# Kernel optimization log

Hardware: AMD Instinct MI355X
Metric: run time of the kernel (lower is better)

Reference implementation:

```python
import jax, jax.numpy as jnp
import numpy as np

NEG = -9e15
SLOPE = 0.1  # LeakyReLU negative_slope in the torch module

B, N, NFEAT = 4, 2048, 256
NHID, NHEADS, NOUT = 64, 8, 128


def setup_inputs() -> dict:
    key = jax.random.key(0)
    ks = jax.random.split(key, 8)
    x = jax.random.normal(ks[0], (B, N, NFEAT), dtype=jnp.float32)
    adj = jax.random.randint(ks[1], (B, N, N), 0, 2, dtype=jnp.int32)
    s = 0.1
    Wh = jax.random.normal(ks[2], (NHEADS, NFEAT, NHID), dtype=jnp.float32) * s
    ah = jax.random.normal(ks[3], (NHEADS, 2 * NHID), dtype=jnp.float32) * s
    bh = jax.random.normal(ks[4], (NHEADS, NHID), dtype=jnp.float32) * s
    Wo = jax.random.normal(ks[5], (NHID * NHEADS, NOUT), dtype=jnp.float32) * s
    ao = jax.random.normal(ks[6], (2 * NOUT,), dtype=jnp.float32) * s
    bo = jax.random.normal(ks[7], (NOUT,), dtype=jnp.float32) * s
    return {"x": x, "adj": adj, "Wh": Wh, "ah": ah, "bh": bh,
            "Wo": Wo, "ao": ao, "bo": bo}


def _leaky(v):
    return jnp.where(v >= 0, v, SLOPE * v)


def _gat_layer(x, adj, W, a, b):
    # x: [B,N,Fin], W: [Fin,F], a: [2F], b: [F]
    h = jnp.einsum('bnf,fo->bno', x, W)          # [B,N,F]
    F = W.shape[1]
    a1, a2 = a[:F], a[F:]
    s1 = h @ a1                                   # [B,N] (query / row term)
    s2 = h @ a2                                   # [B,N] (key / col term)
    e = _leaky(s1[:, :, None] + s2[:, None, :])   # [B,N,N], avoids a_input blowup
    e = jnp.where(adj > 0, e, NEG)
    att = jax.nn.softmax(e, axis=2)               # [B,N,N]
    h_prime = jnp.einsum('bnm,bmf->bnf', att, h) + b
    return jax.nn.elu(h_prime)


def reference(x, adj, Wh, ah, bh, Wo, ao, bo):
    # per-head layers, vmapped over the head axis of the stacked params
    heads = jax.vmap(lambda W, a, b: _gat_layer(x, adj, W, a, b))(Wh, ah, bh)
    # [H,B,N,F] -> concat heads along feature dim: [B,N,H*F]
    hcat = jnp.transpose(heads, (1, 2, 0, 3)).reshape(x.shape[0], x.shape[1], -1)
    out = _gat_layer(hcat, adj, Wo, ao, bo)
    return jax.nn.relu(out)
```

## Files before the change

### kernel.cpp

```cpp
#include <hip/hip_runtime.h>

constexpr int B_ = 4;
constexpr int N_ = 2048;
constexpr int NFEAT_ = 256;
constexpr int NHEADS_ = 8;
constexpr float SLOPE_ = 0.1f;
constexpr float L2E = 1.4426950408889634f;

typedef __attribute__((ext_vector_type(8))) __fp16 f16x8;
typedef __attribute__((ext_vector_type(4))) __fp16 f16x4;
typedef __attribute__((ext_vector_type(2))) __fp16 f16x2;
typedef __attribute__((ext_vector_type(4))) float f32x4;

__device__ __forceinline__ f16x8 pack8(const float* v) {
  union { f16x2 h2[4]; f16x8 h8; } u;
  u.h2[0] = __builtin_amdgcn_cvt_pkrtz(v[0], v[1]);
  u.h2[1] = __builtin_amdgcn_cvt_pkrtz(v[2], v[3]);
  u.h2[2] = __builtin_amdgcn_cvt_pkrtz(v[4], v[5]);
  u.h2[3] = __builtin_amdgcn_cvt_pkrtz(v[6], v[7]);
  return u.h8;
}
__device__ __forceinline__ f16x4 pack4(float a, float b, float c, float d) {
  union { f16x2 h2[2]; f16x4 h4; } u;
  u.h2[0] = __builtin_amdgcn_cvt_pkrtz(a, b);
  u.h2[1] = __builtin_amdgcn_cvt_pkrtz(c, d);
  return u.h4;
}

__global__ __launch_bounds__(256) void k_prep(
    const int* __restrict__ adj, unsigned short* __restrict__ mask2,
    const float* __restrict__ Wh, __fp16* __restrict__ WhB,
    const float* __restrict__ Wo, __fp16* __restrict__ WoB)
{
  const int bid = blockIdx.x;
  const int l = threadIdx.x & 63;
  if (bid < 4096) {
    const size_t gw = ((size_t)bid * 256 + threadIdx.x) >> 6;
    const int jt = (int)(gw & 31);
    const int ig16 = (int)((gw >> 5) & 127);
    const int b = (int)(gw >> 12);
    const int q = l >> 4, c15 = l & 15;
    const int* base = adj + ((size_t)b * N_ + ig16 * 16) * N_ + jt * 64 + l;
    unsigned int msk = 0;
    #pragma unroll
    for (int r = 0; r < 16; ++r) {
      int a = base[(size_t)r * N_];
      unsigned long long bal = __ballot(a > 0);
      unsigned int v = (unsigned int)((bal >> (q * 8)) & 0xffull)
                     | ((unsigned int)((bal >> (q * 8 + 32)) & 0xffull) << 8);
      if (r == c15) msk = v;
    }
    mask2[gw * 64 + l] = (unsigned short)msk;
  } else if (bid < 4160) {
    int s = (int)(((bid - 4096) * 256 + threadIdx.x) >> 6);
    int h = s >> 5, ks = (s >> 2) & 7, ft = s & 3;
    const float* src = Wh + ((size_t)h * 256 + ks * 32 + (l >> 4) * 8) * 64 + ft * 16 + (l & 15);
    float v[8];
    #pragma unroll
    for (int j = 0; j < 8; ++j) v[j] = src[(size_t)j * 64];
    *(f16x8*)(WhB + (size_t)s * 512 + l * 8) = pack8(v);
  } else {
    int s = (int)(((bid - 4160) * 256 + threadIdx.x) >> 6);
    int ks = s >> 3, ft = s & 7;
    const float* src = Wo + ((size_t)ks * 32 + (l >> 4) * 8) * 128 + ft * 16 + (l & 15);
    float v[8];
    #pragma unroll
    for (int j = 0; j < 8; ++j) v[j] = src[(size_t)j * 128];
    *(f16x8*)(WoB + (size_t)s * 512 + l * 8) = pack8(v);
  }
}

__global__ __launch_bounds__(256, 4) void k_gemm1(
    const float* __restrict__ x, const __fp16* __restrict__ WhB,
    const float* __restrict__ ah,
    __fp16* __restrict__ hB1, float* __restrict__ s1h, float* __restrict__ s2h)
{
  constexpr int XP = 264;
  __shared__ __fp16 xs[16 * XP];
  __shared__ __fp16 hT[512 * 16];

  const int t = threadIdx.x;
  const int bid = blockIdx.x;
  const int b = bid >> 7;
  const int n0 = (bid & 127) * 16;

  {
    int r = t >> 4, k0 = (t & 15) * 16;
    const float* src = x + ((size_t)(b * N_) + n0 + r) * NFEAT_ + k0;
    float v0[8], v1[8];
    *(float4*)&v0[0] = *(const float4*)(src);
    *(float4*)&v0[4] = *(const float4*)(src + 4);
    *(float4*)&v1[0] = *(const float4*)(src + 8);
    *(float4*)&v1[4] = *(const float4*)(src + 12);
    *(f16x8*)&xs[r * XP + k0] = pack8(v0);
    *(f16x8*)&xs[r * XP + k0 + 8] = pack8(v1);
  }
  __syncthreads();

  const int w = t >> 6, l = t & 63;
  const int quad = l >> 4, c15 = l & 15;

  f32x4 acc[8];
  #pragma unroll
  for (int i = 0; i < 8; ++i) acc[i] = (f32x4){0.f, 0.f, 0.f, 0.f};

  for (int ks = 0; ks < 8; ++ks) {
    f16x8 af = *(const f16x8*)&xs[c15 * XP + ks * 32 + quad * 8];
    #pragma unroll
    for (int tt = 0; tt < 8; ++tt) {
      int hl = tt >> 2, ft = tt & 3;
      f16x8 bf = *(const f16x8*)(WhB +
          ((((size_t)(2 * w + hl) * 8 + ks) * 4 + ft) * 512) + l * 8);
      acc[tt] = __builtin_amdgcn_mfma_f32_16x16x32_f16(af, bf, acc[tt], 0, 0, 0);
    }
  }

  #pragma unroll
  for (int hl = 0; hl < 2; ++hl) {
    int head = 2 * w + hl;
    float a1v[4], a2v[4];
    #pragma unroll
    for (int ft = 0; ft < 4; ++ft) {
      a1v[ft] = ah[head * 128 + ft * 16 + c15] * L2E;
      a2v[ft] = ah[head * 128 + 64 + ft * 16 + c15] * L2E;
    }
    #pragma unroll
    for (int r = 0; r < 4; ++r) {
      float v1 = 0.f, v2 = 0.f;
      #pragma unroll
      for (int ft = 0; ft < 4; ++ft) {
        v1 = fmaf(acc[hl * 4 + ft][r], a1v[ft], v1);
        v2 = fmaf(acc[hl * 4 + ft][r], a2v[ft], v2);
      }
      #pragma unroll
      for (int off = 1; off < 16; off <<= 1) {
        v1 += __shfl_xor(v1, off, 64);
        v2 += __shfl_xor(v2, off, 64);
      }
      if (c15 == 0) {
        s1h[(size_t)(b * NHEADS_ + head) * N_ + n0 + quad * 4 + r] = v1;
        s2h[(size_t)(b * NHEADS_ + head) * N_ + n0 + quad * 4 + r] = v2;
      }
    }
  }

  #pragma unroll
  for (int tt = 0; tt < 8; ++tt) {
    int f = (2 * w + (tt >> 2)) * 64 + (tt & 3) * 16 + c15;
    *(f16x4*)&hT[f * 16 + quad * 4] =
        pack4(acc[tt][0], acc[tt][1], acc[tt][2], acc[tt][3]);
  }
  __syncthreads();

  const int base_oct = (n0 >> 3) & 3;
  #pragma unroll
  for (int q = 0; q < 4; ++q) {
    int s = t + q * 256;
    int c15v = s & 15, oct = (s >> 4) & 1, ft = (s >> 5) & 3, head = s >> 7;
    f16x8 v = *(const f16x8*)&hT[(head * 64 + ft * 16 + c15v) * 16 + oct * 8];
    int lane0 = (base_oct + oct) * 16 + c15v;
    *(f16x8*)(hB1 +
        ((((size_t)(b * NHEADS_ + head) * 64 + (n0 >> 5)) * 4 + ft) * 512) + lane0 * 8) = v;
  }
}

__global__ __launch_bounds__(256, 4) void k_gemm2(
    const __fp16* __restrict__ g1, const __fp16* __restrict__ WoB,
    const float* __restrict__ ao,
    __fp16* __restrict__ hB2, float* __restrict__ s1o, float* __restrict__ s2o)
{
  constexpr int GP = 520;
  __shared__ __fp16 gs[16 * GP];
  __shared__ __fp16 hT[128 * 16];
  __shared__ float sd1[4][16], sd2[4][16];

  const int t = threadIdx.x;
  const int bid = blockIdx.x;
  const int b = bid >> 7;
  const int n0 = (bid & 127) * 16;

  {
    int r = t >> 4, k0 = (t & 15) * 32;
    const __fp16* src = g1 + ((size_t)(b * N_) + n0 + r) * 512 + k0;
    #pragma unroll
    for (int i = 0; i < 4; ++i)
      *(f16x8*)&gs[r * GP + k0 + i * 8] = *(const f16x8*)(src + i * 8);
  }
  __syncthreads();

  const int w = t >> 6, l = t & 63;
  const int quad = l >> 4, c15 = l & 15;

  f32x4 acc[2];
  acc[0] = (f32x4){0.f, 0.f, 0.f, 0.f};
  acc[1] = (f32x4){0.f, 0.f, 0.f, 0.f};

  for (int ks = 0; ks < 16; ++ks) {
    f16x8 af = *(const f16x8*)&gs[c15 * GP + ks * 32 + quad * 8];
    #pragma unroll
    for (int tt = 0; tt < 2; ++tt) {
      int ft = 2 * w + tt;
      f16x8 bf = *(const f16x8*)(WoB + (((size_t)ks * 8 + ft) * 512) + l * 8);
      acc[tt] = __builtin_amdgcn_mfma_f32_16x16x32_f16(af, bf, acc[tt], 0, 0, 0);
    }
  }

  {
    float a1v[2], a2v[2];
    #pragma unroll
    for (int tt = 0; tt < 2; ++tt) {
      int f = (2 * w + tt) * 16 + c15;
      a1v[tt] = ao[f] * L2E;
      a2v[tt] = ao[128 + f] * L2E;
    }
    #pragma unroll
    for (int r = 0; r < 4; ++r) {
      float v1 = acc[0][r] * a1v[0] + acc[1][r] * a1v[1];
      float v2 = acc[0][r] * a2v[0] + acc[1][r] * a2v[1];
      #pragma unroll
      for (int off = 1; off < 16; off <<= 1) {
        v1 += __shfl_xor(v1, off, 64);
        v2 += __shfl_xor(v2, off, 64);
      }
      if (c15 == 0) { sd1[w][quad * 4 + r] = v1; sd2[w][quad * 4 + r] = v2; }
    }
  }

  #pragma unroll
  for (int tt = 0; tt < 2; ++tt) {
    int f = (2 * w + tt) * 16 + c15;
    *(f16x4*)&hT[f * 16 + quad * 4] =
        pack4(acc[tt][0], acc[tt][1], acc[tt][2], acc[tt][3]);
  }
  __syncthreads();

  if (t < 16)
    s1o[(size_t)b * N_ + n0 + t] = sd1[0][t] + sd1[1][t] + sd1[2][t] + sd1[3][t];
  else if (t < 32) {
    int rr = t - 16;
    s2o[(size_t)b * N_ + n0 + rr] = sd2[0][rr] + sd2[1][rr] + sd2[2][rr] + sd2[3][rr];
  }

  {
    int c15v = t & 15, oct = (t >> 4) & 1, ft = t >> 5;
    f16x8 v = *(const f16x8*)&hT[(ft * 16 + c15v) * 16 + oct * 8];
    int base_oct = (n0 >> 3) & 3;
    int lane0 = (base_oct + oct) * 16 + c15v;
    *(f16x8*)(hB2 +
        (((size_t)(b * 64 + (n0 >> 5)) * 8 + ft) * 512) + lane0 * 8) = v;
  }
}

__global__ __launch_bounds__(512, 4) void k_att1(
    const __fp16* __restrict__ hB, const float* __restrict__ s1,
    const float* __restrict__ s2, const unsigned short* __restrict__ mask2,
    const float* __restrict__ bias, __fp16* __restrict__ g1)
{
  constexpr int NRG = 4, NJQ = 2, JLEN = 1024, TJ = 64, NIT = JLEN / TJ;
  constexpr int TILE = TJ * 64;

  __shared__ __fp16 vbuf[NJQ][2][TILE];
  __shared__ float s2s[N_];
  __shared__ float red[8];

  const int tid = threadIdx.x;
  const int w = tid >> 6, l = tid & 63;
  const int quad = l >> 4, c15 = l & 15;
  const int rowg = w % NRG, jq = w / NRG;
  const int tc = rowg * 64 + l;

  int idx = blockIdx.x;
  const int ig = idx & 31; idx >>= 5;
  const int head = idx & 7;
  const int b = idx >> 3;
  const int i0w = ig * 64 + rowg * 16;

  const float* s1p = s1 + (size_t)(b * 8 + head) * N_;
  const float* s2p = s2 + (size_t)(b * 8 + head) * N_;
  const char* hBp = (const char*)(hB + (size_t)(b * 8 + head) * (N_ / 32) * 2048);
  const unsigned short* mp = mask2 + ((size_t)(b * 128 + (i0w >> 4)) * 32) * 64 + l;

  const int jbase = jq * JLEN;

  auto stage = [&](int j0, int slot) {
    const char* srcb = hBp + (size_t)(j0 >> 5) * 4096;
    #pragma unroll
    for (int c = 0; c < 2; ++c) {
      int off = (tc + c * 256) * 16;
      __builtin_amdgcn_global_load_lds(
          (const __attribute__((address_space(1))) unsigned int*)(srcb + off),
          (__attribute__((address_space(3))) unsigned int*)
              ((char*)&vbuf[jq][slot][0] + (off - l * 16)), 16, 0, 0);
    }
  };

  stage(jbase, 0);
  unsigned int mk = mp[(size_t)(jbase >> 6) * 64];

  float4 sv = *(const float4*)(s2p + tid * 4);
  *(float4*)&s2s[tid * 4] = sv;
  float lm = fmaxf(fmaxf(sv.x, sv.y), fmaxf(sv.z, sv.w));
  #pragma unroll
  for (int off = 1; off < 64; off <<= 1) lm = fmaxf(lm, __shfl_xor(lm, off, 64));
  if (l == 0) red[w] = lm;
  const float s1v = s1p[i0w + c15];
  __syncthreads();
  float s2m = red[0];
  #pragma unroll
  for (int q = 1; q < 8; ++q) s2m = fmaxf(s2m, red[q]);

  const float zm = s1v + s2m;
  const float m = fmaxf(zm, SLOPE_ * zm);
  const float p = s1v - m;
  const float cq = (SLOPE_ - 1.f) * m;

  f16x8 ones;
  #pragma unroll
  for (int i = 0; i < 8; ++i) ones[i] = (__fp16)1.0f;

  f32x4 acc[4], acc5;
  #pragma unroll
  for (int t = 0; t < 4; ++t) acc[t] = (f32x4){0.f, 0.f, 0.f, 0.f};
  acc5 = (f32x4){0.f, 0.f, 0.f, 0.f};

  for (int it = 0; it < NIT; ++it) {
    const int cur = it & 1;
    const int j0 = jbase + it * TJ;
    unsigned int nk = 0;
    if (it + 1 < NIT) {
      stage(j0 + TJ, cur ^ 1);
      nk = mp[(size_t)((j0 + TJ) >> 6) * 64];
    }

    #pragma unroll
    for (int h = 0; h < 2; ++h) {
      const int jk = j0 + h * 32;
      float s2r[8];
      *(float4*)&s2r[0] = *(const float4*)&s2s[jk + quad * 8];
      *(float4*)&s2r[4] = *(const float4*)&s2s[jk + quad * 8 + 4];
      const unsigned int mbyte = (mk >> (8 * h)) & 0xffu;
      float wgt[8];
      #pragma unroll
      for (int k = 0; k < 8; ++k) {
        float t0 = p + s2r[k];
        float t1 = fmaf(SLOPE_, t0, cq);
        float tm = fmaxf(t0, t1);
        float e = __builtin_amdgcn_exp2f(tm);
        int sel = (int)(mbyte << (31 - k)) >> 31;
        union { float f; int i; } u; u.f = e; u.i &= sel;
        wgt[k] = u.f;
      }
      f16x8 a = pack8(wgt);
      acc5 = __builtin_amdgcn_mfma_f32_16x16x32_f16(a, ones, acc5, 0, 0, 0);
      const __fp16* vb = &vbuf[jq][cur][h * 2048];
      #pragma unroll
      for (int t = 0; t < 4; ++t) {
        f16x8 bf = *(const f16x8*)(vb + t * 512 + l * 8);
        acc[t] = __builtin_amdgcn_mfma_f32_16x16x32_f16(a, bf, acc[t], 0, 0, 0);
      }
    }
    mk = nk;
    __syncthreads();
  }

  auto pacc = (float(*)[16][64])(&vbuf[0][0][0]);
  auto pls  = (float(*)[16])(&s2s[0]);
  if (jq == 1) {
    #pragma unroll
    for (int t = 0; t < 4; ++t)
      #pragma unroll
      for (int r = 0; r < 4; ++r)
        pacc[rowg][quad * 4 + r][t * 16 + c15] = acc[t][r];
    if (c15 == 0) {
      #pragma unroll
      for (int r = 0; r < 4; ++r) pls[rowg][quad * 4 + r] = acc5[r];
    }
  }
  __syncthreads();
  if (jq == 0) {
    float Lrow[4];
    #pragma unroll
    for (int r = 0; r < 4; ++r)
      Lrow[r] = acc5[r] + pls[rowg][quad * 4 + r];
    #pragma unroll
    for (int t = 0; t < 4; ++t)
      #pragma unroll
      for (int r = 0; r < 4; ++r)
        acc[t][r] += pacc[rowg][quad * 4 + r][t * 16 + c15];
    float lr[4];
    #pragma unroll
    for (int r = 0; r < 4; ++r) lr[r] = 1.f / Lrow[r];
    #pragma unroll
    for (int t = 0; t < 4; ++t) {
      const float bv = bias[head * 64 + t * 16 + c15];
      #pragma unroll
      for (int r = 0; r < 4; ++r) {
        const int i = i0w + quad * 4 + r;
        float v = acc[t][r] * lr[r] + bv;
        v = (v > 0.f) ? v : expm1f(v);
        g1[(size_t)(b * N_ + i) * 512 + head * 64 + t * 16 + c15] = (__fp16)v;
      }
    }
  }
}

__global__ __launch_bounds__(512, 4) void k_att2(
    const __fp16* __restrict__ hB, const float* __restrict__ s1,
    const float* __restrict__ s2, const unsigned short* __restrict__ mask2,
    const float* __restrict__ bias, float* __restrict__ out)
{
  constexpr int NRG = 2, NJQ = 4, JLEN = 512, TJ = 32, NIT = JLEN / TJ;
  constexpr int TILE = TJ * 64;

  __shared__ __fp16 vbuf[NJQ][2][TILE];
  __shared__ float s2s[N_];
  __shared__ float red[8];

  const int tid = threadIdx.x;
  const int w = tid >> 6, l = tid & 63;
  const int quad = l >> 4, c15 = l & 15;
  const int rowg = w % NRG, jq = w / NRG;
  const int tc = rowg * 64 + l;

  int idx = blockIdx.x;
  const int ig = idx & 63; idx >>= 6;
  const int fs = idx & 1;
  const int b = idx >> 1;
  const int i0w = ig * 32 + rowg * 16;

  const float* s1p = s1 + (size_t)b * N_;
  const float* s2p = s2 + (size_t)b * N_;
  const char* hBp = (const char*)(hB + (size_t)b * 64 * 4096 + fs * 2048);
  const unsigned short* mp = mask2 + ((size_t)(b * 128 + (i0w >> 4)) * 32) * 64 + l;

  const int jbase = jq * JLEN;

  auto stage = [&](int j0, int slot) {
    const char* srcb = hBp + (size_t)(j0 >> 5) * 8192;
    #pragma unroll
    for (int c = 0; c < 2; ++c) {
      int off = (tc + c * 128) * 16;
      __builtin_amdgcn_global_load_lds(
          (const __attribute__((address_space(1))) unsigned int*)(srcb + off),
          (__attribute__((address_space(3))) unsigned int*)
              ((char*)&vbuf[jq][slot][0] + (off - l * 16)), 16, 0, 0);
    }
  };

  stage(jbase, 0);
  unsigned int mk = mp[(size_t)(jbase >> 6) * 64];

  float4 sv = *(const float4*)(s2p + tid * 4);
  *(float4*)&s2s[tid * 4] = sv;
  float lm = fmaxf(fmaxf(sv.x, sv.y), fmaxf(sv.z, sv.w));
  #pragma unroll
  for (int off = 1; off < 64; off <<= 1) lm = fmaxf(lm, __shfl_xor(lm, off, 64));
  if (l == 0) red[w] = lm;
  const float s1v = s1p[i0w + c15];
  __syncthreads();
  float s2m = red[0];
  #pragma unroll
  for (int q = 1; q < 8; ++q) s2m = fmaxf(s2m, red[q]);

  const float zm = s1v + s2m;
  const float m = fmaxf(zm, SLOPE_ * zm);
  const float p = s1v - m;
  const float cq = (SLOPE_ - 1.f) * m;

  f16x8 ones;
  #pragma unroll
  for (int i = 0; i < 8; ++i) ones[i] = (__fp16)1.0f;

  f32x4 acc[4], acc5;
  #pragma unroll
  for (int t = 0; t < 4; ++t) acc[t] = (f32x4){0.f, 0.f, 0.f, 0.f};
  acc5 = (f32x4){0.f, 0.f, 0.f, 0.f};

  for (int it = 0; it < NIT; ++it) {
    const int cur = it & 1;
    const int j0 = jbase + it * TJ;
    unsigned int nk = 0;
    if (it + 1 < NIT) {
      stage(j0 + TJ, cur ^ 1);
      nk = mp[(size_t)((j0 + TJ) >> 6) * 64];
    }

    float s2r[8];
    *(float4*)&s2r[0] = *(const float4*)&s2s[j0 + quad * 8];
    *(float4*)&s2r[4] = *(const float4*)&s2s[j0 + quad * 8 + 4];
    const unsigned int mbyte = (mk >> (8 * ((j0 >> 5) & 1))) & 0xffu;
    float wgt[8];
    #pragma unroll
    for (int k = 0; k < 8; ++k) {
      float t0 = p + s2r[k];
      float t1 = fmaf(SLOPE_, t0, cq);
      float tm = fmaxf(t0, t1);
      float e = __builtin_amdgcn_exp2f(tm);
      int sel = (int)(mbyte << (31 - k)) >> 31;
      union { float f; int i; } u; u.f = e; u.i &= sel;
      wgt[k] = u.f;
    }
    f16x8 a = pack8(wgt);
    acc5 = __builtin_amdgcn_mfma_f32_16x16x32_f16(a, ones, acc5, 0, 0, 0);
    const __fp16* vb = &vbuf[jq][cur][0];
    #pragma unroll
    for (int t = 0; t < 4; ++t) {
      f16x8 bf = *(const f16x8*)(vb + t * 512 + l * 8);
      acc[t] = __builtin_amdgcn_mfma_f32_16x16x32_f16(a, bf, acc[t], 0, 0, 0);
    }
    mk = nk;
    __syncthreads();
  }

  auto pacc = (float(*)[NRG][16][64])(&vbuf[0][0][0]);
  auto pls  = (float(*)[NRG][16])(&s2s[0]);
  if (jq > 0) {
    #pragma unroll
    for (int t = 0; t < 4; ++t)
      #pragma unroll
      for (int r = 0; r < 4; ++r)
        pacc[jq - 1][rowg][quad * 4 + r][t * 16 + c15] = acc[t][r];
    if (c15 == 0) {
      #pragma unroll
      for (int r = 0; r < 4; ++r) pls[jq - 1][rowg][quad * 4 + r] = acc5[r];
    }
  }
  __syncthreads();
  if (jq == 0) {
    float Lrow[4];
    #pragma unroll
    for (int r = 0; r < 4; ++r) Lrow[r] = acc5[r];
    #pragma unroll
    for (int q = 0; q < NJQ - 1; ++q) {
      #pragma unroll
      for (int t = 0; t < 4; ++t)
        #pragma unroll
        for (int r = 0; r < 4; ++r)
          acc[t][r] += pacc[q][rowg][quad * 4 + r][t * 16 + c15];
      #pragma unroll
      for (int r = 0; r < 4; ++r) Lrow[r] += pls[q][rowg][quad * 4 + r];
    }
    float lr[4];
    #pragma unroll
    for (int r = 0; r < 4; ++r) lr[r] = 1.f / Lrow[r];
    #pragma unroll
    for (int t = 0; t < 4; ++t) {
      const float bv = bias[fs * 64 + t * 16 + c15];
      #pragma unroll
      for (int r = 0; r < 4; ++r) {
        const int i = i0w + quad * 4 + r;
        float v = acc[t][r] * lr[r] + bv;
        out[(size_t)(b * N_ + i) * 128 + fs * 64 + t * 16 + c15] = fmaxf(v, 0.f);
      }
    }
  }
}

extern "C" void kernel_launch(void* const* d_in, const int* in_sizes, int n_in,
                              void* d_out, int out_size, void* d_ws, size_t ws_size,
                              hipStream_t stream) {
  const float* x   = (const float*)d_in[0];
  const int*   adj = (const int*)d_in[1];
  const float* Wh  = (const float*)d_in[2];
  const float* ah  = (const float*)d_in[3];
  const float* bh  = (const float*)d_in[4];
  const float* Wo  = (const float*)d_in[5];
  const float* ao  = (const float*)d_in[6];
  const float* bo  = (const float*)d_in[7];
  float* out = (float*)d_out;

  float* ws   = (float*)d_ws;
  float* s1h  = ws;
  float* s2h  = s1h  + (size_t)B_ * NHEADS_ * N_;
  float* s1o  = s2h  + (size_t)B_ * NHEADS_ * N_;
  float* s2o  = s1o  + (size_t)B_ * N_;
  __fp16* g1  = (__fp16*)(s2o + (size_t)B_ * N_);
  __fp16* hB1 = g1  + (size_t)B_ * N_ * 512;
  __fp16* hB2 = hB1 + (size_t)B_ * NHEADS_ * N_ * 64;
  __fp16* WhB = hB2 + (size_t)B_ * N_ * 128;
  __fp16* WoB = WhB + (size_t)8 * 256 * 64;
  unsigned short* mask2 = (unsigned short*)(WoB + (size_t)512 * 128);

  k_prep<<<4192, 256, 0, stream>>>(adj, mask2, Wh, WhB, Wo, WoB);
  k_gemm1<<<B_ * (N_ / 16), 256, 0, stream>>>(x, WhB, ah, hB1, s1h, s2h);
  k_att1<<<B_ * NHEADS_ * (N_ / 64), 512, 0, stream>>>(
      hB1, s1h, s2h, mask2, bh, g1);
  k_gemm2<<<B_ * (N_ / 16), 256, 0, stream>>>(g1, WoB, ao, hB2, s1o, s2o);
  k_att2<<<B_ * 2 * (N_ / 32), 512, 0, stream>>>(
      hB2, s1o, s2o, mask2, bo, out);
}
```

Baseline: 195.5 us.

## Drop LDS s2 staging, remap blocks per XCD, use exp2 for ELU

Both attention kernels stop copying the s2 score vector into shared memory and read it straight from global memory, relying on L1/L2 caching. This shrinks LDS use per block, which may allow more blocks per CU. Block indices are remapped so the low three bits pick the XCD and each XCD handles one batch and half the heads or feature slices, to keep hB and mask data local to that XCD's L2. The ELU expm1f is replaced by exp2(v*log2e)-1, which is cheaper but loses precision for small negative values.

```diff
diff --git a/kernel.cpp b/kernel.cpp
--- a/kernel.cpp
+++ b/kernel.cpp
@@ -260,8 +260,8 @@
   constexpr int TILE = TJ * 64;
 
   __shared__ __fp16 vbuf[NJQ][2][TILE];
-  __shared__ float s2s[N_];
   __shared__ float red[8];
+  __shared__ float pls[NRG][16];
 
   const int tid = threadIdx.x;
   const int w = tid >> 6, l = tid & 63;
@@ -269,10 +269,12 @@
   const int rowg = w % NRG, jq = w / NRG;
   const int tc = rowg * 64 + l;
 
-  int idx = blockIdx.x;
-  const int ig = idx & 31; idx >>= 5;
-  const int head = idx & 7;
-  const int b = idx >> 3;
+  const int bid = blockIdx.x;
+  const int xcd = bid & 7;
+  const int q7 = bid >> 3;
+  const int b = xcd >> 1;
+  const int head = (xcd & 1) * 4 + (q7 >> 5);
+  const int ig = q7 & 31;
   const int i0w = ig * 64 + rowg * 16;
 
   const float* s1p = s1 + (size_t)(b * 8 + head) * N_;
@@ -298,7 +300,6 @@
   unsigned int mk = mp[(size_t)(jbase >> 6) * 64];
 
   float4 sv = *(const float4*)(s2p + tid * 4);
-  *(float4*)&s2s[tid * 4] = sv;
   float lm = fmaxf(fmaxf(sv.x, sv.y), fmaxf(sv.z, sv.w));
   #pragma unroll
   for (int off = 1; off < 64; off <<= 1) lm = fmaxf(lm, __shfl_xor(lm, off, 64));
@@ -336,8 +337,8 @@
     for (int h = 0; h < 2; ++h) {
       const int jk = j0 + h * 32;
       float s2r[8];
-      *(float4*)&s2r[0] = *(const float4*)&s2s[jk + quad * 8];
-      *(float4*)&s2r[4] = *(const float4*)&s2s[jk + quad * 8 + 4];
+      *(float4*)&s2r[0] = *(const float4*)(s2p + jk + quad * 8);
+      *(float4*)&s2r[4] = *(const float4*)(s2p + jk + quad * 8 + 4);
       const unsigned int mbyte = (mk >> (8 * h)) & 0xffu;
       float wgt[8];
       #pragma unroll
@@ -364,7 +365,6 @@
   }
 
   auto pacc = (float(*)[16][64])(&vbuf[0][0][0]);
-  auto pls  = (float(*)[16])(&s2s[0]);
   if (jq == 1) {
     #pragma unroll
     for (int t = 0; t < 4; ++t)
@@ -397,7 +397,7 @@
       for (int r = 0; r < 4; ++r) {
         const int i = i0w + quad * 4 + r;
         float v = acc[t][r] * lr[r] + bv;
-        v = (v > 0.f) ? v : expm1f(v);
+        v = (v > 0.f) ? v : (__builtin_amdgcn_exp2f(v * L2E) - 1.0f);
         g1[(size_t)(b * N_ + i) * 512 + head * 64 + t * 16 + c15] = (__fp16)v;
       }
     }
@@ -413,8 +413,8 @@
   constexpr int TILE = TJ * 64;
 
   __shared__ __fp16 vbuf[NJQ][2][TILE];
-  __shared__ float s2s[N_];
   __shared__ float red[8];
+  __shared__ float pls[NJQ - 1][NRG][16];
 
   const int tid = threadIdx.x;
   const int w = tid >> 6, l = tid & 63;
@@ -422,10 +422,11 @@
   const int rowg = w % NRG, jq = w / NRG;
   const int tc = rowg * 64 + l;
 
-  int idx = blockIdx.x;
-  const int ig = idx & 63; idx >>= 6;
-  const int fs = idx & 1;
-  const int b = idx >> 1;
+  const int bid = blockIdx.x;
+  const int xcd = bid & 7;
+  const int b = xcd >> 1;
+  const int fs = xcd & 1;
+  const int ig = bid >> 3;
   const int i0w = ig * 32 + rowg * 16;
 
   const float* s1p = s1 + (size_t)b * N_;
@@ -451,7 +452,6 @@
   unsigned int mk = mp[(size_t)(jbase >> 6) * 64];
 
   float4 sv = *(const float4*)(s2p + tid * 4);
-  *(float4*)&s2s[tid * 4] = sv;
   float lm = fmaxf(fmaxf(sv.x, sv.y), fmaxf(sv.z, sv.w));
   #pragma unroll
   for (int off = 1; off < 64; off <<= 1) lm = fmaxf(lm, __shfl_xor(lm, off, 64));
@@ -486,8 +486,8 @@
     }
 
     float s2r[8];
-    *(float4*)&s2r[0] = *(const float4*)&s2s[j0 + quad * 8];
-    *(float4*)&s2r[4] = *(const float4*)&s2s[j0 + quad * 8 + 4];
+    *(float4*)&s2r[0] = *(const float4*)(s2p + j0 + quad * 8);
+    *(float4*)&s2r[4] = *(const float4*)(s2p + j0 + quad * 8 + 4);
     const unsigned int mbyte = (mk >> (8 * ((j0 >> 5) & 1))) & 0xffu;
     float wgt[8];
     #pragma unroll
@@ -513,7 +513,6 @@
   }
 
   auto pacc = (float(*)[NRG][16][64])(&vbuf[0][0][0]);
-  auto pls  = (float(*)[NRG][16])(&s2s[0]);
   if (jq > 0) {
     #pragma unroll
     for (int t = 0; t < 4; ++t)
```

Measured after the change: 202.9 us. 1.04x slower.
